# Optimization experiments

Hardware: AMD Instinct MI355X
Metric: run time of the kernel (lower is better)

The kernel has to match this reference:

```python
import jax, jax.numpy as jnp
import numpy as np

ZERO = -1e4  # Semiring.zero (finite log-zero, as in the torch repo)


def semiring_eye(n, dtype=jnp.float32):
    # log-semiring identity: 0 on diagonal, ZERO off-diagonal
    return jnp.where(jnp.eye(n, dtype=bool), jnp.zeros((), dtype), jnp.full((), ZERO, dtype))


def log_bmm(a, b):
    # LogSemiring.bmm: out[..., i, j] = logsumexp_k(a[..., i, k] + b[..., k, j])
    # matmul-based stable form: avoids materializing the [..., i, k, j] tensor
    am = jnp.max(a, axis=-1, keepdims=True)          # [..., i, 1]
    bm = jnp.max(b, axis=-2, keepdims=True)          # [..., 1, j]
    return am + bm + jnp.log(jnp.matmul(jnp.exp(a - am), jnp.exp(b - bm)))


def crf_reduce(potentials):
    # tree-doubling scan, faithful to reduce() in the torch source
    B, L, T, _ = potentials.shape
    n = L.bit_length()
    pad = (1 << n) - L
    eye = jnp.broadcast_to(semiring_eye(T, potentials.dtype), (B, pad, T, T))
    p = jnp.concatenate([potentials, eye], axis=1)
    for _ in range(n):
        p = log_bmm(p[:, 0::2], p[:, 1::2])
    return p[:, 0]  # [B, T, T]


def setup_inputs() -> dict:
    key = jax.random.key(0)
    k1, k2, k3, k4 = jax.random.split(key, 4)
    B, L, T = 32, 1024, 64
    logits = jax.random.normal(k1, (B, L, T), jnp.float32)
    mask = jnp.ones((B, L), dtype=bool)
    # xavier_normal_ for square matrix: std = sqrt(2 / (T + T))
    transitions = jax.random.normal(k2, (T, T), jnp.float32) * np.sqrt(2.0 / (T + T)).astype(np.float32)
    start_states = jax.random.normal(k3, (T,), jnp.float32)
    end_states = jax.random.normal(k4, (T,), jnp.float32)
    return {"logits": logits, "transitions": transitions,
            "start_states": start_states, "end_states": end_states, "mask": mask}


def reference(logits, transitions, start_states, end_states, mask):
    B, L, T = logits.shape
    end_idx = jnp.sum(mask, axis=-1) - 1                      # [B]
    # include_start: add start_states to first step
    logits = logits.at[:, 0].add(start_states)
    # include_end: scatter-add end_states at last unmasked step
    logits = logits.at[jnp.arange(B), end_idx].add(end_states)
    # zero out padded positions
    logits = logits * mask[..., None]
    me = mask[:, 1:, None, None]                              # [B, L-1, 1, 1]
    trans = transitions[None, None] * me                      # [B, L-1, T, T]
    # LogSemiring.mul == add
    pot = logits[:, 1:, None, :] + trans                      # [B, L-1, T, T]
    pot = pot * me + semiring_eye(T, logits.dtype) * (~me)
    red = crf_reduce(pot)                                     # [B, T, T]
    red = red + logits[:, 0][..., None]                       # start_potentials[..., None]
    return jax.nn.logsumexp(red, axis=(-1, -2))               # [B] log-partition
```

## Files before the change

kernel.cpp:

```cpp
#include <hip/hip_runtime.h>
#include <hip/hip_bf16.h>

typedef __attribute__((ext_vector_type(8))) short short8;
typedef __attribute__((ext_vector_type(4))) float floatx4;
typedef __attribute__((ext_vector_type(4))) unsigned int uint4v;
typedef __attribute__((ext_vector_type(2))) unsigned int uint2v;

#define L_SEQ    1024
#define N_BATCH  32
#define CHUNKA   128
#define NCHUNKA  8
#define REC_SH   4096
#define MST      72

__device__ __forceinline__ unsigned short f2bf(float f) {
    unsigned u = __builtin_bit_cast(unsigned, f);
    return (unsigned short)((u + 0x8000u) >> 16);
}
__device__ __forceinline__ float bf2f(unsigned short h) {
    return __builtin_bit_cast(float, ((unsigned)h) << 16);
}
__device__ __forceinline__ unsigned pkbf(float hi, float lo) {
    unsigned uh = __builtin_bit_cast(unsigned, hi) + 0x8000u;
    unsigned ul = __builtin_bit_cast(unsigned, lo) + 0x8000u;
    return __builtin_amdgcn_perm(uh, ul, 0x07060302u);
}

__device__ __forceinline__ void gload_lds16(const void* g, void* l) {
    __builtin_amdgcn_global_load_lds(
        (const __attribute__((address_space(1))) void*)g,
        (__attribute__((address_space(3))) void*)l, 16, 0, 0);
}

__device__ __forceinline__ int rec_idx(int n, int u) {
    return n * 64 + (u ^ (n & 7)) * 8;
}

__device__ __forceinline__ short8 ldA(const unsigned short* rec, int n, int h, int q) {
    const int u0 = 4 * h + (q >> 1), sub = (q & 1) * 4;
    uint2v lo = *(const uint2v*)(rec + n * 64 + ((u0 ^ (n & 7)) * 8) + sub);
    uint2v hi = *(const uint2v*)(rec + n * 64 + (((u0 + 2) ^ (n & 7)) * 8) + sub);
    uint4v r = {lo[0], lo[1], hi[0], hi[1]};
    return __builtin_bit_cast(short8, r);
}

#define MFMA16(A, B, C) __builtin_amdgcn_mfma_f32_16x16x32_bf16((A), (B), (C), 0, 0, 0)

__global__ __launch_bounds__(256, 4) void crf_phaseA(
    const float* __restrict__ logits, const float* __restrict__ trans,
    const float* __restrict__ end_states, unsigned short* __restrict__ wsA,
    float* __restrict__ sclA)
{
    __shared__ __align__(16) unsigned short Me[64 * MST];
    __shared__ __align__(16) float LdsE[CHUNKA * 64];
    __shared__ float offs[4];

    const int tid = threadIdx.x, lane = tid & 63, w = tid >> 6;
    const int q = lane >> 4, c = lane & 15, R0 = w * 16;
    const int b = blockIdx.y, chunk = blockIdx.x;

    const int l0 = 1 + chunk * CHUNKA;
    const int isTail = (chunk == NCHUNKA - 1);
    const int stageBase = l0 - (isTail ? 1 : 0);
    const int nsteps = isTail ? (L_SEQ - l0) : CHUNKA;

    {
        const float* gsrc = logits + (size_t)b * L_SEQ * 64 + (size_t)stageBase * 64;
        #pragma unroll
        for (int i = 0; i < 8; ++i) {
            const int ch = 8 * w + i;
            gload_lds16(gsrc + ch * 256 + lane * 4, &LdsE[ch * 256]);
        }
    }

    short8 bfr[4][2];
    #pragma unroll
    for (int t = 0; t < 4; ++t) {
        #pragma unroll
        for (int h = 0; h < 2; ++h) {
            short8 v;
            #pragma unroll
            for (int j = 0; j < 8; ++j) {
                const int kk = (2 * h + (j >> 2)) * 16 + q * 4 + (j & 3);
                v[j] = (short)f2bf(__expf(trans[kk * 64 + t * 16 + c]));
            }
            bfr[t][h] = v;
        }
    }
    __syncthreads();

    for (int i = tid; i < CHUNKA * 64 / 4; i += 256) {
        floatx4 v = ((floatx4*)LdsE)[i];
        if (stageBase + (i >> 4) == L_SEQ - 1) {
            const int j0 = (i & 15) * 4;
            #pragma unroll
            for (int e = 0; e < 4; ++e) v[e] += end_states[j0 + e];
        }
        #pragma unroll
        for (int e = 0; e < 4; ++e) v[e] = __expf(v[e]);
        ((floatx4*)LdsE)[i] = v;
    }
    __syncthreads();

    unsigned P[8];
    #pragma unroll
    for (int t = 0; t < 4; ++t) {
        float h0 = (t * 16 + q * 4 + 0 == R0 + c) ? 1.f : 0.f;
        float h1 = (t * 16 + q * 4 + 1 == R0 + c) ? 1.f : 0.f;
        float h2 = (t * 16 + q * 4 + 2 == R0 + c) ? 1.f : 0.f;
        float h3 = (t * 16 + q * 4 + 3 == R0 + c) ? 1.f : 0.f;
        P[2 * t]     = pkbf(h1, h0);
        P[2 * t + 1] = pkbf(h3, h2);
    }

    float off = 0.f;

    auto stepf = [&](int li, bool renorm) {
        floatx4 ewv[4];
        #pragma unroll
        for (int t = 0; t < 4; ++t)
            ewv[t] = *(const floatx4*)&LdsE[li * 64 + t * 16 + q * 4];

        const short8 b0 = __builtin_bit_cast(short8, (uint4v){P[0], P[1], P[2], P[3]});
        const short8 b1 = __builtin_bit_cast(short8, (uint4v){P[4], P[5], P[6], P[7]});

        float h[4][4];
        #pragma unroll
        for (int t = 0; t < 4; ++t) {
            floatx4 z = {0.f, 0.f, 0.f, 0.f};
            z = MFMA16(bfr[t][0], b0, z);
            z = MFMA16(bfr[t][1], b1, z);
            #pragma unroll
            for (int r = 0; r < 4; ++r) h[t][r] = z[r] * ewv[t][r];
        }

        if (renorm) {
            float m = h[0][0];
            #pragma unroll
            for (int t = 0; t < 4; ++t)
                #pragma unroll
                for (int r = 0; r < 4; ++r) m = fmaxf(m, h[t][r]);
            #pragma unroll
            for (int d = 32; d >= 1; d >>= 1) m = fmaxf(m, __shfl_xor(m, d, 64));
            m = fmaxf(m, 1e-30f);
            float inv = __builtin_amdgcn_rcpf(m);
            off += __logf(m);
            #pragma unroll
            for (int t = 0; t < 4; ++t)
                #pragma unroll
                for (int r = 0; r < 4; ++r) h[t][r] *= inv;
        }

        #pragma unroll
        for (int t = 0; t < 4; ++t) {
            P[2 * t]     = pkbf(h[t][1], h[t][0]);
            P[2 * t + 1] = pkbf(h[t][3], h[t][2]);
        }
    };

    const int liBase = l0 - stageBase;
    if (!isTail) {
        for (int g = 0; g < CHUNKA / 8; ++g) {
            #pragma unroll
            for (int k = 0; k < 8; ++k)
                stepf(liBase + g * 8 + k, k == 7);
        }
    } else {
        for (int s = 0; s < nsteps; ++s)
            stepf(liBase + s, ((s & 7) == 7) || (s == nsteps - 1));
    }

    {
        unsigned short* wrow = &Me[(R0 + c) * MST];
        #pragma unroll
        for (int t = 0; t < 4; ++t) {
            uint2v d = {P[2 * t], P[2 * t + 1]};
            *(uint2v*)(wrow + t * 16 + q * 4) = d;
        }
    }
    if (lane == 0) offs[w] = off;
    __syncthreads();

    float omax = fmaxf(fmaxf(offs[0], offs[1]), fmaxf(offs[2], offs[3]));
    const int rid = b * NCHUNKA + chunk;
    unsigned short* rec = wsA + (size_t)rid * REC_SH;
    const int n = tid & 63, qq = tid >> 6;
    float eo = __expf(offs[qq] - omax);
    unsigned short tmp[16] __attribute__((aligned(16)));
    #pragma unroll
    for (int r = 0; r < 16; ++r)
        tmp[r] = f2bf(bf2f(Me[(qq * 16 + r) * MST + n]) * eo);
    *(uint4v*)(rec + rec_idx(n, 2 * qq))     = *(uint4v*)(tmp);
    *(uint4v*)(rec + rec_idx(n, 2 * qq + 1)) = *(uint4v*)(tmp + 8);
    if (tid == 0) sclA[rid] = omax;
}

template<int NSTEPS, int NSTAGE>
__global__ __launch_bounds__(256) void crf_final(
    const unsigned short* __restrict__ inRecs, const float* __restrict__ sclIn,
    const float* __restrict__ logits, const float* __restrict__ start_states,
    float* __restrict__ out)
{
    __shared__ __align__(16) unsigned short stage[NSTAGE][REC_SH];
    __shared__ __align__(16) unsigned short Me[64 * MST];
    __shared__ float offs[4];
    __shared__ float es[64];
    __shared__ float redA;
    __shared__ float wsum[4];

    const int tid = threadIdx.x, lane = tid & 63, w = tid >> 6;
    const int q = lane >> 4, c = lane & 15, R0 = w * 16;
    const int b = blockIdx.y;
    const int recBase = b * NSTEPS;

    #pragma unroll
    for (int r = 0; r < NSTAGE; ++r) {
        const unsigned short* src = inRecs + (size_t)(recBase + r) * REC_SH;
        #pragma unroll
        for (int i = 0; i < 2; ++i) {
            const int ch = 2 * w + i;
            gload_lds16(src + ch * 512 + lane * 8, &stage[r][ch * 512]);
        }
    }

    float sstep[NSTEPS];
    #pragma unroll
    for (int s = 0; s < NSTEPS; ++s) sstep[s] = sclIn[recBase + s];

    unsigned P[8];
    #pragma unroll
    for (int t = 0; t < 4; ++t) {
        float h0 = (t * 16 + q * 4 + 0 == R0 + c) ? 1.f : 0.f;
        float h1 = (t * 16 + q * 4 + 1 == R0 + c) ? 1.f : 0.f;
        float h2 = (t * 16 + q * 4 + 2 == R0 + c) ? 1.f : 0.f;
        float h3 = (t * 16 + q * 4 + 3 == R0 + c) ? 1.f : 0.f;
        P[2 * t]     = pkbf(h1, h0);
        P[2 * t + 1] = pkbf(h3, h2);
    }

    __syncthreads();

    float off = 0.f;
    #pragma unroll
    for (int s = 0; s < NSTEPS; ++s) {
        if (NSTEPS > NSTAGE) {
            if (s == 2) {
                __syncthreads();
                #pragma unroll
                for (int r = 0; r < NSTEPS - NSTAGE; ++r) {
                    const unsigned short* src =
                        inRecs + (size_t)(recBase + NSTAGE + r) * REC_SH;
                    #pragma unroll
                    for (int i = 0; i < 2; ++i) {
                        const int ch = 2 * w + i;
                        gload_lds16(src + ch * 512 + lane * 8, &stage[r][ch * 512]);
                    }
                }
            }
            if (s == NSTAGE) __syncthreads();
        }
        const unsigned short* rec = stage[(s < NSTAGE) ? s : (s - NSTAGE)];
        off += sstep[s];

        const short8 b0 = __builtin_bit_cast(short8, (uint4v){P[0], P[1], P[2], P[3]});
        const short8 b1 = __builtin_bit_cast(short8, (uint4v){P[4], P[5], P[6], P[7]});

        float h[4][4];
        #pragma unroll
        for (int t = 0; t < 4; ++t) {
            const int n = t * 16 + c;
            short8 a0 = ldA(rec, n, 0, q);
            short8 a1 = ldA(rec, n, 1, q);
            floatx4 z = {0.f, 0.f, 0.f, 0.f};
            z = MFMA16(a0, b0, z);
            z = MFMA16(a1, b1, z);
            #pragma unroll
            for (int r = 0; r < 4; ++r) h[t][r] = z[r];
        }

        #pragma unroll
        for (int t = 0; t < 4; ++t) {
            P[2 * t]     = pkbf(h[t][1], h[t][0]);
            P[2 * t + 1] = pkbf(h[t][3], h[t][2]);
        }
    }

    {
        unsigned short* wrow = &Me[(R0 + c) * MST];
        #pragma unroll
        for (int t = 0; t < 4; ++t) {
            uint2v d = {P[2 * t], P[2 * t + 1]};
            *(uint2v*)(wrow + t * 16 + q * 4) = d;
        }
    }
    if (lane == 0) offs[w] = off;
    __syncthreads();

    if (w == 0) {
        float u = offs[lane >> 4] + logits[(size_t)b * L_SEQ * 64 + lane]
                  + start_states[lane];
        float A1 = u;
        #pragma unroll
        for (int d = 32; d >= 1; d >>= 1) A1 = fmaxf(A1, __shfl_xor(A1, d, 64));
        es[lane] = __expf(u - A1);
        if (lane == 0) redA = A1;
    }
    __syncthreads();
    const int i = tid >> 2, jb = (tid & 3) * 16;
    float sum = 0.f;
    #pragma unroll
    for (int j = 0; j < 16; ++j) sum += bf2f(Me[i * MST + jb + j]);
    sum *= es[i];
    #pragma unroll
    for (int d = 32; d >= 1; d >>= 1) sum += __shfl_xor(sum, d, 64);
    if (lane == 0) wsum[w] = sum;
    __syncthreads();
    if (tid == 0)
        out[b] = redA + __logf(wsum[0] + wsum[1] + wsum[2] + wsum[3]);
}

extern "C" void kernel_launch(void* const* d_in, const int* in_sizes, int n_in,
                              void* d_out, int out_size, void* d_ws, size_t ws_size,
                              hipStream_t stream)
{
    const float* logits       = (const float*)d_in[0];
    const float* trans        = (const float*)d_in[1];
    const float* start_states = (const float*)d_in[2];
    const float* end_states   = (const float*)d_in[3];

    unsigned short* wsA = (unsigned short*)d_ws;
    float* sclA = (float*)(wsA + (size_t)N_BATCH * NCHUNKA * REC_SH);
    float* out  = (float*)d_out;

    crf_phaseA<<<dim3(NCHUNKA, N_BATCH), 256, 0, stream>>>(
        logits, trans, end_states, wsA, sclA);
    crf_final<8, 6><<<dim3(1, N_BATCH), 256, 0, stream>>>(
        wsA, sclA, logits, start_states, out);
}
```

Measured before the change: 104.4 us.

## Halve phase-A chunk length, doubling chunks, and stage all records in final kernel

```diff
diff --git a/kernel.cpp b/kernel.cpp
--- a/kernel.cpp
+++ b/kernel.cpp
@@ -8,8 +8,8 @@
 
 #define L_SEQ    1024
 #define N_BATCH  32
-#define CHUNKA   128
-#define NCHUNKA  8
+#define CHUNKA   64
+#define NCHUNKA  16
 #define REC_SH   4096
 #define MST      72
 
@@ -67,8 +67,8 @@
     {
         const float* gsrc = logits + (size_t)b * L_SEQ * 64 + (size_t)stageBase * 64;
         #pragma unroll
-        for (int i = 0; i < 8; ++i) {
-            const int ch = 8 * w + i;
+        for (int i = 0; i < 4; ++i) {
+            const int ch = 4 * w + i;
             gload_lds16(gsrc + ch * 256 + lane * 4, &LdsE[ch * 256]);
         }
     }
@@ -195,13 +195,13 @@
     if (tid == 0) sclA[rid] = omax;
 }
 
-template<int NSTEPS, int NSTAGE>
+template<int NSTEPS>
 __global__ __launch_bounds__(256) void crf_final(
     const unsigned short* __restrict__ inRecs, const float* __restrict__ sclIn,
     const float* __restrict__ logits, const float* __restrict__ start_states,
     float* __restrict__ out)
 {
-    __shared__ __align__(16) unsigned short stage[NSTAGE][REC_SH];
+    __shared__ __align__(16) unsigned short stage[NSTEPS][REC_SH];
     __shared__ __align__(16) unsigned short Me[64 * MST];
     __shared__ float offs[4];
     __shared__ float es[64];
@@ -214,7 +214,7 @@
     const int recBase = b * NSTEPS;
 
     #pragma unroll
-    for (int r = 0; r < NSTAGE; ++r) {
+    for (int r = 0; r < NSTEPS; ++r) {
         const unsigned short* src = inRecs + (size_t)(recBase + r) * REC_SH;
         #pragma unroll
         for (int i = 0; i < 2; ++i) {
@@ -243,23 +243,7 @@
     float off = 0.f;
     #pragma unroll
     for (int s = 0; s < NSTEPS; ++s) {
-        if (NSTEPS > NSTAGE) {
-            if (s == 2) {
-                __syncthreads();
-                #pragma unroll
-                for (int r = 0; r < NSTEPS - NSTAGE; ++r) {
-                    const unsigned short* src =
-                        inRecs + (size_t)(recBase + NSTAGE + r) * REC_SH;
-                    #pragma unroll
-                    for (int i = 0; i < 2; ++i) {
-                        const int ch = 2 * w + i;
-                        gload_lds16(src + ch * 512 + lane * 8, &stage[r][ch * 512]);
-                    }
-                }
-            }
-            if (s == NSTAGE) __syncthreads();
-        }
-        const unsigned short* rec = stage[(s < NSTAGE) ? s : (s - NSTAGE)];
+        const unsigned short* rec = stage[s];
         off += sstep[s];
 
         const short8 b0 = __builtin_bit_cast(short8, (uint4v){P[0], P[1], P[2], P[3]});
@@ -276,6 +260,23 @@
             z = MFMA16(a1, b1, z);
             #pragma unroll
             for (int r = 0; r < 4; ++r) h[t][r] = z[r];
+        }
+
+        if (s == 7) {
+            float m = h[0][0];
+            #pragma unroll
+            for (int t = 0; t < 4; ++t)
+                #pragma unroll
+                for (int r = 0; r < 4; ++r) m = fmaxf(m, h[t][r]);
+            #pragma unroll
+            for (int d = 32; d >= 1; d >>= 1) m = fmaxf(m, __shfl_xor(m, d, 64));
+            m = fmaxf(m, 1e-30f);
+            float inv = __builtin_amdgcn_rcpf(m);
+            off += __logf(m);
+            #pragma unroll
+            for (int t = 0; t < 4; ++t)
+                #pragma unroll
+                for (int r = 0; r < 4; ++r) h[t][r] *= inv;
         }
 
         #pragma unroll
@@ -334,6 +335,6 @@
 
     crf_phaseA<<<dim3(NCHUNKA, N_BATCH), 256, 0, stream>>>(
         logits, trans, end_states, wsA, sclA);
-    crf_final<8, 6><<<dim3(1, N_BATCH), 256, 0, stream>>>(
+    crf_final<NCHUNKA><<<dim3(1, N_BATCH), 256, 0, stream>>>(
         wsA, sclA, logits, start_states, out);
 }
```

Result: faster. 94.45 us (-9.5%).
